# Performance work log

Measured on AMD Instinct MI355X. Metric: run time of the kernel, lower is better.

The kernel has to match this reference:

```python
import math
import jax, jax.numpy as jnp
import numpy as np

N, D, K = 8192, 256, 32


def setup_inputs() -> dict:
    key = jax.random.key(0)
    kx, kw, kb = jax.random.split(key, 3)
    x = jax.random.normal(kx, (N, D), dtype=jnp.float32)
    # params per _init_weights: w ~ N(1, 0.01), b ~ N(0, 0.01)
    w = 1.0 + 0.01 * jax.random.normal(kw, (K, D), dtype=jnp.float32)
    b = 0.01 * jax.random.normal(kb, (K, D), dtype=jnp.float32)
    return {"x": x, "w": w, "b": b}


def reference(x, w, b):
    # x: (N, D); w, b: (K, D)
    y1 = w[None, :, :] * (x[:, None, :] + b[None, :, :])        # (N, K, D)
    y2 = y1 * y1                                                 # (N, K, D)
    y4 = -0.5 * jnp.sum(y2, axis=-1)                             # (N, K)
    gamma = jax.nn.softmax(y4, axis=-1)                          # (N, K)
    y6 = (y2 - 1.0) * (1.0 / math.sqrt(2.0))                     # (N, K, D)
    g = gamma[:, :, None]                                        # (N, K, 1)
    n, kk, d = y1.shape
    sigma_part = (g * y6).reshape(n, kk * d)                     # (N, K*D)
    mu_part = (g * y1).reshape(n, kk * d)                        # (N, K*D)
    phi_patches = jnp.concatenate([sigma_part, mu_part], axis=-1)
    return jnp.mean(phi_patches, axis=0)                         # (2*K*D,)
```

## Files before the change

### kernel.cpp

```cpp
#include <hip/hip_runtime.h>
#include <math.h>

#define Nn 8192
#define Dd 256
#define Kk 32

typedef float f4x __attribute__((ext_vector_type(4)));

#define P_OFF   0
#define P2_OFF  4194304
#define SP_OFF  4325376

__global__ __launch_bounds__(1024) void fused_kernel(const float* __restrict__ x,
                                                     const float* __restrict__ w,
                                                     const float* __restrict__ b,
                                                     float* __restrict__ ws) {
    __shared__ __align__(16) float4 uS4[64 * 33];
    __shared__ __align__(16) float4 vS4[64 * 33];
    __shared__ __align__(16) float4 xS4[32 * 64];
    __shared__ float  gS[1024];

    float* P  = ws + P_OFF;
    float* Sp = ws + SP_OFF;
    int tid = threadIdx.x;
    int blk = blockIdx.x;

    {
        const float* xg = x + (size_t)blk * 32 * Dd;
        #pragma unroll
        for (int i = 0; i < 2; ++i) {
            int e4 = tid + i * 1024;
            __builtin_amdgcn_global_load_lds(
                (const __attribute__((address_space(1))) void*)(xg + (size_t)e4 * 4),
                (__attribute__((address_space(3))) void*)(&xS4[e4]),
                16, 0, 0);
        }
    }

    {
        const float4* w4 = (const float4*)w;
        const float4* b4 = (const float4*)b;
        #pragma unroll
        for (int i = 0; i < 2; ++i) {
            int e4 = tid + i * 1024;
            int k  = e4 >> 6;
            int d4 = e4 & 63;
            float4 wv = w4[e4];
            float4 bv = b4[e4];
            float4 vv = {wv.x * bv.x, wv.y * bv.y, wv.z * bv.z, wv.w * bv.w};
            uS4[d4 * 33 + k] = wv;
            vS4[d4 * 33 + k] = vv;
        }
    }
    __syncthreads();

    {
        int lane = tid & 63;
        int wave = tid >> 6;
        int k = lane & 31;
        int h = lane >> 5;
        int r0 = wave * 2;

        const float4* xr0 = &xS4[(r0 + 0) * 64];
        const float4* xr1 = &xS4[(r0 + 1) * 64];

        float4 a0 = {0.f, 0.f, 0.f, 0.f}, a1 = a0;

        #pragma unroll 8
        for (int i = 0; i < 32; ++i) {
            int ii = h * 32 + i;
            float4 u  = uS4[ii * 33 + k];
            float4 v  = vS4[ii * 33 + k];
            float4 x0 = xr0[ii];
            float4 x1 = xr1[ii];
            float y;
            y = fmaf(u.x, x0.x, v.x); a0.x = fmaf(y, y, a0.x);
            y = fmaf(u.y, x0.y, v.y); a0.y = fmaf(y, y, a0.y);
            y = fmaf(u.z, x0.z, v.z); a0.z = fmaf(y, y, a0.z);
            y = fmaf(u.w, x0.w, v.w); a0.w = fmaf(y, y, a0.w);
            y = fmaf(u.x, x1.x, v.x); a1.x = fmaf(y, y, a1.x);
            y = fmaf(u.y, x1.y, v.y); a1.y = fmaf(y, y, a1.y);
            y = fmaf(u.z, x1.z, v.z); a1.z = fmaf(y, y, a1.z);
            y = fmaf(u.w, x1.w, v.w); a1.w = fmaf(y, y, a1.w);
        }

        float s0 = (a0.x + a0.y) + (a0.z + a0.w);
        float s1 = (a1.x + a1.y) + (a1.z + a1.w);
        s0 += __shfl_xor(s0, 32);
        s1 += __shfl_xor(s1, 32);
        float y40 = -0.5f * s0, y41 = -0.5f * s1;

        float m0 = y40, m1 = y41;
        #pragma unroll
        for (int o = 16; o >= 1; o >>= 1) {
            m0 = fmaxf(m0, __shfl_xor(m0, o));
            m1 = fmaxf(m1, __shfl_xor(m1, o));
        }
        float e0 = __expf(y40 - m0), e1 = __expf(y41 - m1);
        float t0 = e0, t1 = e1;
        #pragma unroll
        for (int o = 16; o >= 1; o >>= 1) {
            t0 += __shfl_xor(t0, o);
            t1 += __shfl_xor(t1, o);
        }
        if (h == 0) {
            gS[(r0 + 0) * 32 + k] = e0 / t0;
            gS[(r0 + 1) * 32 + k] = e1 / t1;
        }
    }
    __syncthreads();

    if (tid < 32) {
        float s0 = 0.f, s1 = 0.f, s2 = 0.f, s3 = 0.f;
        #pragma unroll
        for (int r = 0; r < 32; r += 4) {
            s0 += gS[(r + 0) * 32 + tid];
            s1 += gS[(r + 1) * 32 + tid];
            s2 += gS[(r + 2) * 32 + tid];
            s3 += gS[(r + 3) * 32 + tid];
        }
        Sp[tid * 256 + blk] = (s0 + s1) + (s2 + s3);
    }

    {
        int kq = tid >> 8;
        int d  = tid & 255;
        const float* xl = (const float*)xS4;
        const float4* gS4 = (const float4*)gS;

        float aG[8], aH[8];
        #pragma unroll
        for (int j = 0; j < 8; ++j) { aG[j] = 0.f; aH[j] = 0.f; }

        #pragma unroll 4
        for (int r = 0; r < 32; ++r) {
            float xv = xl[r * 256 + d];
            float xx = xv * xv;
            #pragma unroll
            for (int q = 0; q < 2; ++q) {
                float4 gv = gS4[r * 8 + kq * 2 + q];
                aG[4*q+0] = fmaf(gv.x, xv, aG[4*q+0]); aH[4*q+0] = fmaf(gv.x, xx, aH[4*q+0]);
                aG[4*q+1] = fmaf(gv.y, xv, aG[4*q+1]); aH[4*q+1] = fmaf(gv.y, xx, aH[4*q+1]);
                aG[4*q+2] = fmaf(gv.z, xv, aG[4*q+2]); aH[4*q+2] = fmaf(gv.z, xx, aH[4*q+2]);
                aG[4*q+3] = fmaf(gv.w, xv, aG[4*q+3]); aH[4*q+3] = fmaf(gv.w, xx, aH[4*q+3]);
            }
        }

        #pragma unroll
        for (int j = 0; j < 8; ++j) {
            int k = kq * 8 + j;
            __builtin_nontemporal_store(aG[j], &P[((size_t)(k * 2 + 0) * 256 + blk) * 256 + d]);
            __builtin_nontemporal_store(aH[j], &P[((size_t)(k * 2 + 1) * 256 + blk) * 256 + d]);
        }
    }
}

__global__ __launch_bounds__(256) void red1_kernel(float* __restrict__ ws) {
    const f4x* P4  = (const f4x*)(ws + P_OFF);
    f4x*       P24 = (f4x*)(ws + P2_OFF);
    __shared__ __align__(16) f4x sS[256];
    int tid = threadIdx.x;
    int c4  = tid & 63;
    int g   = tid >> 6;

    const f4x* p = P4 + ((size_t)blockIdx.x * 32 + g * 8) * 64 + c4;
    f4x a0 = {0.f, 0.f, 0.f, 0.f}, a1 = a0;
    #pragma unroll
    for (int i = 0; i < 8; i += 2) {
        f4x v0 = __builtin_nontemporal_load(&p[(size_t)(i + 0) * 64]);
        f4x v1 = __builtin_nontemporal_load(&p[(size_t)(i + 1) * 64]);
        a0 += v0;
        a1 += v1;
    }
    sS[tid] = a0 + a1;
    __syncthreads();

    if (g == 0) {
        f4x out = (sS[c4] + sS[64 + c4]) + (sS[128 + c4] + sS[192 + c4]);
        P24[(size_t)blockIdx.x * 64 + c4] = out;
    }
}

__global__ __launch_bounds__(256) void red2_kernel(const float* __restrict__ w,
                                                   const float* __restrict__ b,
                                                   const float* __restrict__ ws,
                                                   float* __restrict__ out) {
    const float* P2 = ws + P2_OFF;
    const float* Sp = ws + SP_OFF;
    __shared__ float sred[4];
    int k = blockIdx.x, d = threadIdx.x;

    float sv_part = Sp[k * 256 + d];
    #pragma unroll
    for (int o = 32; o >= 1; o >>= 1) sv_part += __shfl_xor(sv_part, o);
    if ((d & 63) == 0) sred[d >> 6] = sv_part;
    __syncthreads();
    float sv = (sred[0] + sred[1]) + (sred[2] + sred[3]);

    const float* pg = P2 + (size_t)(k * 2 + 0) * 8 * 256 + d;
    const float* ph = P2 + (size_t)(k * 2 + 1) * 8 * 256 + d;
    float Gv = 0.f, Hv = 0.f;
    #pragma unroll
    for (int c = 0; c < 8; ++c) {
        Gv += pg[c * 256];
        Hv += ph[c * 256];
    }

    int idx = k * Dd + d;
    float wv = w[idx], bv = b[idx];
    const float invN = 1.0f / 8192.0f;
    const float c2 = 0.70710678118654752440f * invN;
    float mu = wv * (Gv + bv * sv) * invN;
    float w2 = wv * wv;
    float sg = (w2 * (Hv + 2.0f * bv * Gv + bv * bv * sv) - sv) * c2;
    out[idx] = sg;
    out[Kk * Dd + idx] = mu;
}

extern "C" void kernel_launch(void* const* d_in, const int* in_sizes, int n_in,
                              void* d_out, int out_size, void* d_ws, size_t ws_size,
                              hipStream_t stream) {
    const float* x = (const float*)d_in[0];
    const float* w = (const float*)d_in[1];
    const float* b = (const float*)d_in[2];
    float* out = (float*)d_out;
    float* ws = (float*)d_ws;

    hipLaunchKernelGGL(fused_kernel, dim3(256), dim3(1024), 0, stream, x, w, b, ws);
    hipLaunchKernelGGL(red1_kernel,  dim3(512), dim3(256),  0, stream, ws);
    hipLaunchKernelGGL(red2_kernel,  dim3(32),  dim3(256),  0, stream, w, b, ws, out);
}
```

Measured before the change: 79.82 us.

## Merge three kernels into one cooperative kernel with grid syncs

```diff
diff --git a/kernel.cpp b/kernel.cpp
--- a/kernel.cpp
+++ b/kernel.cpp
@@ -1,5 +1,8 @@
 #include <hip/hip_runtime.h>
+#include <hip/hip_cooperative_groups.h>
 #include <math.h>
+
+namespace cg = cooperative_groups;
 
 #define Nn 8192
 #define Dd 256
@@ -11,16 +14,18 @@
 #define P2_OFF  4194304
 #define SP_OFF  4325376
 
-__global__ __launch_bounds__(1024) void fused_kernel(const float* __restrict__ x,
-                                                     const float* __restrict__ w,
-                                                     const float* __restrict__ b,
-                                                     float* __restrict__ ws) {
+__global__ __launch_bounds__(1024) void fused_all(const float* __restrict__ x,
+                                                  const float* __restrict__ w,
+                                                  const float* __restrict__ b,
+                                                  float* __restrict__ ws,
+                                                  float* __restrict__ out) {
     __shared__ __align__(16) float4 uS4[64 * 33];
     __shared__ __align__(16) float4 vS4[64 * 33];
     __shared__ __align__(16) float4 xS4[32 * 64];
     __shared__ float  gS[1024];
 
     float* P  = ws + P_OFF;
+    float* P2 = ws + P2_OFF;
     float* Sp = ws + SP_OFF;
     int tid = threadIdx.x;
     int blk = blockIdx.x;
@@ -36,7 +41,6 @@
                 16, 0, 0);
         }
     }
-
     {
         const float4* w4 = (const float4*)w;
         const float4* b4 = (const float4*)b;
@@ -153,68 +157,68 @@
             __builtin_nontemporal_store(aH[j], &P[((size_t)(k * 2 + 1) * 256 + blk) * 256 + d]);
         }
     }
-}
-
-__global__ __launch_bounds__(256) void red1_kernel(float* __restrict__ ws) {
-    const f4x* P4  = (const f4x*)(ws + P_OFF);
-    f4x*       P24 = (f4x*)(ws + P2_OFF);
-    __shared__ __align__(16) f4x sS[256];
-    int tid = threadIdx.x;
-    int c4  = tid & 63;
-    int g   = tid >> 6;
-
-    const f4x* p = P4 + ((size_t)blockIdx.x * 32 + g * 8) * 64 + c4;
-    f4x a0 = {0.f, 0.f, 0.f, 0.f}, a1 = a0;
-    #pragma unroll
-    for (int i = 0; i < 8; i += 2) {
-        f4x v0 = __builtin_nontemporal_load(&p[(size_t)(i + 0) * 64]);
-        f4x v1 = __builtin_nontemporal_load(&p[(size_t)(i + 1) * 64]);
-        a0 += v0;
-        a1 += v1;
-    }
-    sS[tid] = a0 + a1;
-    __syncthreads();
-
-    if (g == 0) {
-        f4x out = (sS[c4] + sS[64 + c4]) + (sS[128 + c4] + sS[192 + c4]);
-        P24[(size_t)blockIdx.x * 64 + c4] = out;
-    }
-}
-
-__global__ __launch_bounds__(256) void red2_kernel(const float* __restrict__ w,
-                                                   const float* __restrict__ b,
-                                                   const float* __restrict__ ws,
-                                                   float* __restrict__ out) {
-    const float* P2 = ws + P2_OFF;
-    const float* Sp = ws + SP_OFF;
-    __shared__ float sred[4];
-    int k = blockIdx.x, d = threadIdx.x;
-
-    float sv_part = Sp[k * 256 + d];
-    #pragma unroll
-    for (int o = 32; o >= 1; o >>= 1) sv_part += __shfl_xor(sv_part, o);
-    if ((d & 63) == 0) sred[d >> 6] = sv_part;
-    __syncthreads();
-    float sv = (sred[0] + sred[1]) + (sred[2] + sred[3]);
-
-    const float* pg = P2 + (size_t)(k * 2 + 0) * 8 * 256 + d;
-    const float* ph = P2 + (size_t)(k * 2 + 1) * 8 * 256 + d;
-    float Gv = 0.f, Hv = 0.f;
-    #pragma unroll
-    for (int c = 0; c < 8; ++c) {
-        Gv += pg[c * 256];
-        Hv += ph[c * 256];
-    }
-
-    int idx = k * Dd + d;
-    float wv = w[idx], bv = b[idx];
-    const float invN = 1.0f / 8192.0f;
-    const float c2 = 0.70710678118654752440f * invN;
-    float mu = wv * (Gv + bv * sv) * invN;
-    float w2 = wv * wv;
-    float sg = (w2 * (Hv + 2.0f * bv * Gv + bv * bv * sv) - sv) * c2;
-    out[idx] = sg;
-    out[Kk * Dd + idx] = mu;
+
+    cg::this_grid().sync();
+
+    {
+        f4x* sT = (f4x*)uS4;
+        const f4x* P4  = (const f4x*)P;
+        f4x*       P24 = (f4x*)P2;
+        int half = tid >> 9;
+        int t    = blk * 2 + half;
+        int lt   = tid & 511;
+        int c4   = lt & 63;
+        int g    = lt >> 6;
+
+        const f4x* p = P4 + ((size_t)t * 32 + g * 4) * 64 + c4;
+        f4x a0 = __builtin_nontemporal_load(&p[0]);
+        f4x a1 = __builtin_nontemporal_load(&p[64]);
+        a0 += __builtin_nontemporal_load(&p[128]);
+        a1 += __builtin_nontemporal_load(&p[192]);
+        sT[half * 512 + g * 64 + c4] = a0 + a1;
+        __syncthreads();
+
+        if (g == 0) {
+            f4x s = sT[half * 512 + c4];
+            #pragma unroll
+            for (int j = 1; j < 8; ++j) s += sT[half * 512 + j * 64 + c4];
+            P24[(size_t)t * 64 + c4] = s;
+        }
+    }
+
+    cg::this_grid().sync();
+
+    if (blk < 32) {
+        int k = blk;
+        float sv_part = 0.f;
+        if (tid < 256) sv_part = Sp[k * 256 + tid];
+        #pragma unroll
+        for (int o = 32; o >= 1; o >>= 1) sv_part += __shfl_xor(sv_part, o);
+        if (tid < 256 && (tid & 63) == 0) gS[tid >> 6] = sv_part;
+        __syncthreads();
+        if (tid < 256) {
+            int d = tid;
+            float sv = (gS[0] + gS[1]) + (gS[2] + gS[3]);
+            const float* pg = P2 + (size_t)(k * 2 + 0) * 8 * 256 + d;
+            const float* ph = P2 + (size_t)(k * 2 + 1) * 8 * 256 + d;
+            float Gv = 0.f, Hv = 0.f;
+            #pragma unroll
+            for (int c = 0; c < 8; ++c) {
+                Gv += pg[c * 256];
+                Hv += ph[c * 256];
+            }
+
+            int idx = k * Dd + d;
+            float wv = w[idx], bv = b[idx];
+            const float invN = 1.0f / 8192.0f;
+            const float c2 = 0.70710678118654752440f * invN;
+            float mu = wv * (Gv + bv * sv) * invN;
+            float w2 = wv * wv;
+            float sg = (w2 * (Hv + 2.0f * bv * Gv + bv * bv * sv) - sv) * c2;
+            out[idx] = sg;
+            out[Kk * Dd + idx] = mu;
+        }
+    }
 }
 
 extern "C" void kernel_launch(void* const* d_in, const int* in_sizes, int n_in,
@@ -226,7 +230,7 @@
     float* out = (float*)d_out;
     float* ws = (float*)d_ws;
 
-    hipLaunchKernelGGL(fused_kernel, dim3(256), dim3(1024), 0, stream, x, w, b, ws);
-    hipLaunchKernelGGL(red1_kernel,  dim3(512), dim3(256),  0, stream, ws);
-    hipLaunchKernelGGL(red2_kernel,  dim3(32),  dim3(256),  0, stream, w, b, ws, out);
+    void* args[5] = {(void*)&x, (void*)&w, (void*)&b, (void*)&ws, (void*)&out};
+    hipLaunchCooperativeKernel((const void*)fused_all, dim3(256), dim3(1024),
+                               args, 0, stream);
 }
```

Measured after the change: 153.4 us. 1.92x slower.

## Store per-block partial sums as bf16 and vectorize the gamma-weighted accumulation

Applied to the files above, without the earlier changes.

```diff
diff --git a/kernel.cpp b/kernel.cpp
--- a/kernel.cpp
+++ b/kernel.cpp
@@ -5,11 +5,24 @@
 #define Dd 256
 #define Kk 32
 
-typedef float f4x __attribute__((ext_vector_type(4)));
-
-#define P_OFF   0
-#define P2_OFF  4194304
-#define SP_OFF  4325376
+typedef float        f4x __attribute__((ext_vector_type(4)));
+typedef unsigned int u2x __attribute__((ext_vector_type(2)));
+typedef unsigned int u4x __attribute__((ext_vector_type(4)));
+
+#define P2_OFF  2097152
+#define SP_OFF  2228224
+
+__device__ __forceinline__ unsigned bfpack(float a, float b) {
+    unsigned ua = __float_as_uint(a); ua += 0x7FFFu + ((ua >> 16) & 1u);
+    unsigned ub = __float_as_uint(b); ub += 0x7FFFu + ((ub >> 16) & 1u);
+    return (ua >> 16) | (ub & 0xFFFF0000u);
+}
+__device__ __forceinline__ void nt_store_bf4(unsigned short* p, f4x v) {
+    u2x d2; d2.x = bfpack(v.x, v.y); d2.y = bfpack(v.z, v.w);
+    __builtin_nontemporal_store(d2, (u2x*)p);
+}
+__device__ __forceinline__ float bflo(unsigned u) { return __uint_as_float(u << 16); }
+__device__ __forceinline__ float bfhi(unsigned u) { return __uint_as_float(u & 0xFFFF0000u); }
 
 __global__ __launch_bounds__(1024) void fused_kernel(const float* __restrict__ x,
                                                      const float* __restrict__ w,
@@ -20,7 +33,6 @@
     __shared__ __align__(16) float4 xS4[32 * 64];
     __shared__ float  gS[1024];
 
-    float* P  = ws + P_OFF;
     float* Sp = ws + SP_OFF;
     int tid = threadIdx.x;
     int blk = blockIdx.x;
@@ -123,61 +135,61 @@
     }
 
     {
-        int kq = tid >> 8;
-        int d  = tid & 255;
-        const float* xl = (const float*)xS4;
-        const float4* gS4 = (const float4*)gS;
-
-        float aG[8], aH[8];
-        #pragma unroll
-        for (int j = 0; j < 8; ++j) { aG[j] = 0.f; aH[j] = 0.f; }
+        int kg = tid >> 6;
+        int d4 = tid & 63;
+        const f4x* xl4 = (const f4x*)xS4;
+        const float2* gS2 = (const float2*)gS;
+
+        f4x aG0 = {0.f, 0.f, 0.f, 0.f}, aH0 = aG0, aG1 = aG0, aH1 = aG0;
 
         #pragma unroll 4
         for (int r = 0; r < 32; ++r) {
-            float xv = xl[r * 256 + d];
-            float xx = xv * xv;
-            #pragma unroll
-            for (int q = 0; q < 2; ++q) {
-                float4 gv = gS4[r * 8 + kq * 2 + q];
-                aG[4*q+0] = fmaf(gv.x, xv, aG[4*q+0]); aH[4*q+0] = fmaf(gv.x, xx, aH[4*q+0]);
-                aG[4*q+1] = fmaf(gv.y, xv, aG[4*q+1]); aH[4*q+1] = fmaf(gv.y, xx, aH[4*q+1]);
-                aG[4*q+2] = fmaf(gv.z, xv, aG[4*q+2]); aH[4*q+2] = fmaf(gv.z, xx, aH[4*q+2]);
-                aG[4*q+3] = fmaf(gv.w, xv, aG[4*q+3]); aH[4*q+3] = fmaf(gv.w, xx, aH[4*q+3]);
-            }
-        }
-
-        #pragma unroll
-        for (int j = 0; j < 8; ++j) {
-            int k = kq * 8 + j;
-            __builtin_nontemporal_store(aG[j], &P[((size_t)(k * 2 + 0) * 256 + blk) * 256 + d]);
-            __builtin_nontemporal_store(aH[j], &P[((size_t)(k * 2 + 1) * 256 + blk) * 256 + d]);
-        }
+            f4x xv = xl4[r * 64 + d4];
+            f4x xx = xv * xv;
+            float2 g2 = gS2[r * 16 + kg];
+            aG0 += g2.x * xv;  aH0 += g2.x * xx;
+            aG1 += g2.y * xv;  aH1 += g2.y * xx;
+        }
+
+        unsigned short* Pb = (unsigned short*)ws;
+        int k0 = kg * 2, k1 = k0 + 1;
+        size_t dd = (size_t)4 * d4;
+        nt_store_bf4(Pb + ((size_t)(k0 * 2 + 0) * 256 + blk) * 256 + dd, aG0);
+        nt_store_bf4(Pb + ((size_t)(k0 * 2 + 1) * 256 + blk) * 256 + dd, aH0);
+        nt_store_bf4(Pb + ((size_t)(k1 * 2 + 0) * 256 + blk) * 256 + dd, aG1);
+        nt_store_bf4(Pb + ((size_t)(k1 * 2 + 1) * 256 + blk) * 256 + dd, aH1);
     }
 }
 
 __global__ __launch_bounds__(256) void red1_kernel(float* __restrict__ ws) {
-    const f4x* P4  = (const f4x*)(ws + P_OFF);
-    f4x*       P24 = (f4x*)(ws + P2_OFF);
-    __shared__ __align__(16) f4x sS[256];
+    const unsigned short* Pb = (const unsigned short*)ws;
+    f4x* P24 = (f4x*)(ws + P2_OFF);
+    __shared__ __align__(16) f4x sT[512];
     int tid = threadIdx.x;
-    int c4  = tid & 63;
-    int g   = tid >> 6;
-
-    const f4x* p = P4 + ((size_t)blockIdx.x * 32 + g * 8) * 64 + c4;
+    int cb = tid & 31;
+    int g  = tid >> 5;
+
+    const u4x* p = (const u4x*)(Pb + ((size_t)blockIdx.x * 32 + g * 4) * 256 + cb * 8);
     f4x a0 = {0.f, 0.f, 0.f, 0.f}, a1 = a0;
     #pragma unroll
-    for (int i = 0; i < 8; i += 2) {
-        f4x v0 = __builtin_nontemporal_load(&p[(size_t)(i + 0) * 64]);
-        f4x v1 = __builtin_nontemporal_load(&p[(size_t)(i + 1) * 64]);
-        a0 += v0;
-        a1 += v1;
-    }
-    sS[tid] = a0 + a1;
+    for (int j = 0; j < 4; ++j) {
+        u4x v = __builtin_nontemporal_load(&p[(size_t)j * 32]);
+        a0.x += bflo(v.x); a0.y += bfhi(v.x); a0.z += bflo(v.y); a0.w += bfhi(v.y);
+        a1.x += bflo(v.z); a1.y += bfhi(v.z); a1.z += bflo(v.w); a1.w += bfhi(v.w);
+    }
+    sT[(g * 32 + cb) * 2 + 0] = a0;
+    sT[(g * 32 + cb) * 2 + 1] = a1;
     __syncthreads();
 
     if (g == 0) {
-        f4x out = (sS[c4] + sS[64 + c4]) + (sS[128 + c4] + sS[192 + c4]);
-        P24[(size_t)blockIdx.x * 64 + c4] = out;
+        f4x s0 = sT[cb * 2], s1 = sT[cb * 2 + 1];
+        #pragma unroll
+        for (int j = 1; j < 8; ++j) {
+            s0 += sT[(j * 32 + cb) * 2 + 0];
+            s1 += sT[(j * 32 + cb) * 2 + 1];
+        }
+        P24[(size_t)blockIdx.x * 64 + cb * 2 + 0] = s0;
+        P24[(size_t)blockIdx.x * 64 + cb * 2 + 1] = s1;
     }
 }
 
```

Result: faster. 78.02 us (-2.3%).
